# Kernel optimization log

Measured on AMD Instinct MI355X. Metric: run time of the kernel, lower is better.

## Reference

```python
import jax, jax.numpy as jnp
import numpy as np

H = 256; S = 64; AN = 16; D = 8; HH = 8; WW = 8; T = 32; N = 64; NV = 32
HG = 2 + 3 * H  # GRU hidden = sum(parser_sections) = 1 + 1 + 3*H


def _gru(x, w_ih, w_hh, b_ih, b_hh):
    """torch-style GRU over leading axis; x: [L, N, Hin] -> [L, N, HG]."""
    def step(h, xt):
        gi = xt @ w_ih.T + b_ih
        gh = h @ w_hh.T + b_hh
        ir, iz, inn = jnp.split(gi, 3, axis=-1)
        hr, hz, hn = jnp.split(gh, 3, axis=-1)
        r = jax.nn.sigmoid(ir + hr)
        z = jax.nn.sigmoid(iz + hz)
        n = jnp.tanh(inn + r * hn)
        h2 = (1 - z) * n + z * h
        return h2, h2
    h0 = jnp.zeros((x.shape[1], w_hh.shape[1]), x.dtype)
    _, ys = jax.lax.scan(step, h0, x)
    return ys


def _cos(e, m):  # e [N,H], m [N,S,H] -> [N,S]; matches F.cosine_similarity eps=1e-8
    num = jnp.einsum('nh,nsh->ns', e, m)
    den = jnp.linalg.norm(e, axis=-1)[:, None] * jnp.linalg.norm(m, axis=-1)
    return num / jnp.maximum(den, 1e-8)


def _l1norm(x):  # F.normalize(x, p=1, dim=-1)
    return x / jnp.maximum(jnp.abs(x).sum(-1, keepdims=True), 1e-12)


def setup_inputs():
    key = jax.random.key(0)
    ks = jax.random.split(key, 16)
    sc = lambda k, shape, fan: jax.random.normal(k, shape, jnp.float32) / np.float32(np.sqrt(fan))
    return dict(
        base=jax.random.normal(ks[0], (T, N, D, HH, WW), jnp.float32),
        interactable=(jax.random.uniform(ks[1], (T, N, AN - 5)) < 0.5).astype(jnp.float32),
        rnn_hxs=jnp.zeros((1, N, 1 + AN + 1 + H + S), jnp.float32),
        emb=sc(ks[2], (NV, H), 1.0),
        gru_w_ih=sc(ks[3], (3 * HG, H), H),
        gru_w_hh=sc(ks[4], (3 * HG, HG), HG),
        gru_b_ih=jnp.zeros((3 * HG,), jnp.float32),
        gru_b_hh=jnp.zeros((3 * HG,), jnp.float32),
        conv0_w=sc(ks[5], (H, D * H), D * H),
        conv0_b=jnp.zeros((H,), jnp.float32),
        convs_w=sc(ks[6], (2, H, H), H),
        convs_b=jnp.zeros((2, H), jnp.float32),
        lin_w=sc(ks[7], (H, H * HH * WW), H * HH * WW),
        lin_b=jnp.zeros((H,), jnp.float32),
        psi_w=sc(ks[8], (H, H * AN), H * AN),
        psi_b=jnp.zeros((H,), jnp.float32),
        actor_w=sc(ks[9], (AN, H), H),
        actor_b=jnp.zeros((AN,), jnp.float32),
        critic_w=sc(ks[10], (1, H), H),
        critic_b=jnp.zeros((1,), jnp.float32),
        subtasks=jax.random.randint(ks[11], (N, S), 0, NV),
        actions=jax.random.randint(ks[12], (T, N), 0, AN),
    )


def reference(base, interactable, rnn_hxs, emb, gru_w_ih, gru_w_hh, gru_b_ih, gru_b_hh,
              conv0_w, conv0_b, convs_w, convs_b, lin_w, lin_b, psi_w, psi_b,
              actor_w, actor_b, critic_w, critic_b, subtasks, actions):
    # --- parser: GRU over the subtask token sequence ---
    rnn_in = emb[subtasks].transpose(1, 0, 2)                                    # [S, N, H]
    X = _gru(rnn_in, gru_w_ih, gru_w_hh, gru_b_ih, gru_b_hh).transpose(1, 0, 2)  # [N, S, HG]
    c, p0 = X[..., 0], X[..., 1]                                                 # [N, S]
    M = X[..., 2:2 + H]
    Mm = X[..., 2 + H:2 + 2 * H]
    Mp = X[..., 2 + 2 * H:]
    hx = rnn_hxs[0]
    new_ep = jnp.all(rnn_hxs == 0, axis=-1)[0]                                   # [N]
    p_init = jnp.where(new_ep[:, None], p0, hx[:, 1 + AN + 1 + H:])

    def f_net(base_t, r):
        n = base_t.shape[0]
        # outer product [N,H,d,h,w] -> [N, H*d, h, w], then 1x1 convs
        x = (base_t[:, None] * r[:, :, None, None, None]).reshape(n, H * D, HH, WW)
        x = jax.nn.relu(jnp.einsum('nchw,oc->nohw', x, conv0_w) + conv0_b[None, :, None, None])
        for i in range(convs_w.shape[0]):
            x = jax.nn.relu(jnp.einsum('nchw,oc->nohw', x, convs_w[i]) + convs_b[i][None, :, None, None])
        return jax.nn.relu(x.reshape(n, -1) @ lin_w.T + lin_b)

    def step(p, xs):
        base_t, inter_t, a_t = xs
        ps = jax.nn.softmax(p, axis=-1)
        r = jnp.einsum('ns,nsh->nh', ps, M)                                      # memory read
        s = f_net(base_t, r)
        dprobs = jax.nn.softmax(s @ actor_w.T + actor_b, axis=-1)
        nonzero = jnp.pad(inter_t, ((0, 0), (5, 0)), constant_values=1.0)        # [N, AN]
        probs = dprobs * nonzero
        deficit = 1.0 - probs.sum(-1, keepdims=True)
        probs = probs + _l1norm(nonzero) * deficit
        probs = _l1norm(jnp.clip(probs, 0.0, 1.0))
        a_oh = jax.nn.one_hot(a_t, AN, dtype=s.dtype)
        e = (s[:, :, None] * a_oh[:, None, :]).reshape(s.shape[0], H * AN) @ psi_w.T + psi_b
        p_new = ps + c * _cos(e, Mp) - c * _cos(e, Mm)                           # memory write
        v = s @ critic_w.T + critic_b
        out = jnp.concatenate([a_t[:, None].astype(s.dtype), probs, v, s, p_new], axis=-1)
        return p_new, out

    _, hx_out = jax.lax.scan(step, p_init, (base, interactable, actions))        # [T, N, 338]
    return hx_out, hx_out[-1:]
```

## Files before the change

kernel.cpp:

```cpp
#include <hip/hip_runtime.h>
#include <math.h>

constexpr int cH  = 256;
constexpr int cS  = 64;
constexpr int cAN = 16;
constexpr int cD  = 8;
constexpr int cT  = 32;
constexpr int cN  = 64;
constexpr int cHG = 770;
constexpr int cG3 = 2310;
constexpr int cOW = 338;
constexpr int XLD = 800;
constexpr int GLD = 832;
constexpr int MLD = 2496;

__global__ __launch_bounds__(256) void k_gitab(const float* __restrict__ emb,
                                               const float* __restrict__ w_ih,
                                               const float* __restrict__ b_ih,
                                               float* __restrict__ gitp) {
  int v = blockIdx.y;
  int j = blockIdx.x * 256 + threadIdx.x;
  __shared__ float es[cH];
  es[threadIdx.x] = emb[v * cH + threadIdx.x];
  __syncthreads();
  if (j < cG3) {
    float acc = b_ih[j];
    const float* wr = w_ih + (size_t)j * cH;
    #pragma unroll 8
    for (int h = 0; h < cH; ++h) acc += wr[h] * es[h];
    int g = j / cHG, kk = j - g * cHG;
    gitp[(size_t)v * MLD + g * GLD + kk] = acc;
  }
}

__global__ __launch_bounds__(256) void k_wpad(const float* __restrict__ whh,
                                              float* __restrict__ wpadG) {
  int idx = blockIdx.x * 256 + threadIdx.x;
  if (idx < MLD * XLD) {
    int row = idx / XLD, col = idx - row * XLD;
    int g = row / GLD, k = row - g * GLD;
    wpadG[idx] = (k < cHG && col < cHG) ? whh[(size_t)(g * cHG + k) * cHG + col] : 0.f;
  }
}

__global__ __launch_bounds__(256) void k_psiperm(const float* __restrict__ psi_w,
                                                 float* __restrict__ psip) {
  int idx = blockIdx.x * 256 + threadIdx.x;
  int a = idx >> 16, h = (idx >> 8) & 255, o = idx & 255;
  psip[idx] = psi_w[((size_t)o * cH + h) * cAN + a];
}

__global__ __launch_bounds__(256) void k_gru_gemm(const float* __restrict__ wpadG,
                                                  const float* __restrict__ X,
                                                  float* __restrict__ part, int s) {
  int tid = threadIdx.x;
  int tile = blockIdx.x % 39;
  int ks   = blockIdx.x / 39;
  int g = tile / 13, kt = tile - g * 13;
  int cbase = (ks <= 2) ? ks * 13 : 38;
  int ccnt  = (ks < 2) ? 13 : 12;
  int kbase = cbase * 16;
  int csz = ccnt * 16;

  __shared__ float Bst[208][68];
  __shared__ float As[2][16][68];

  const float* bsrc = wpadG + ((size_t)(g * GLD + kt * 64)) * XLD + kbase;
  for (int i = tid; i < 64 * 208; i += 256) {
    int jl = i / 208, k2l = i - jl * 208;
    if (k2l < csz) Bst[k2l][jl] = bsrc[(size_t)jl * XLD + k2l];
  }

  int tm = tid & 15, tj = tid >> 4;
  int lrow = tid >> 2, lcol = (tid & 3) * 4;
  __syncthreads();

  float acc[4][4] = {};
  const float* Xp = X + ((size_t)lrow * cS + (s - 1)) * XLD + kbase;
  float4 av = *(const float4*)(Xp + lcol);
  for (int c = 0; c < ccnt; ++c) {
    int buf = c & 1;
    As[buf][lcol + 0][lrow] = av.x;
    As[buf][lcol + 1][lrow] = av.y;
    As[buf][lcol + 2][lrow] = av.z;
    As[buf][lcol + 3][lrow] = av.w;
    __syncthreads();
    if (c + 1 < ccnt) av = *(const float4*)(Xp + (c + 1) * 16 + lcol);
    #pragma unroll
    for (int kk = 0; kk < 16; ++kk) {
      float4 a4 = *(const float4*)&As[buf][kk][tm * 4];
      float4 b4 = *(const float4*)&Bst[c * 16 + kk][tj * 4];
      acc[0][0] += a4.x * b4.x; acc[0][1] += a4.x * b4.y; acc[0][2] += a4.x * b4.z; acc[0][3] += a4.x * b4.w;
      acc[1][0] += a4.y * b4.x; acc[1][1] += a4.y * b4.y; acc[1][2] += a4.y * b4.z; acc[1][3] += a4.y * b4.w;
      acc[2][0] += a4.z * b4.x; acc[2][1] += a4.z * b4.y; acc[2][2] += a4.z * b4.z; acc[2][3] += a4.z * b4.w;
      acc[3][0] += a4.w * b4.x; acc[3][1] += a4.w * b4.y; acc[3][2] += a4.w * b4.z; acc[3][3] += a4.w * b4.w;
    }
    __syncthreads();
  }
  float* pw = part + (size_t)ks * (64 * MLD) + (size_t)(g * GLD + kt * 64);
  #pragma unroll
  for (int i = 0; i < 4; ++i) {
    *(float4*)(pw + (size_t)(tm * 4 + i) * MLD + tj * 4) =
        make_float4(acc[i][0], acc[i][1], acc[i][2], acc[i][3]);
  }
}

__global__ __launch_bounds__(256) void k_gru_gate(const float* __restrict__ part,
                                                  const float* __restrict__ bhh,
                                                  const float* __restrict__ gitp,
                                                  const int* __restrict__ subtasks,
                                                  float* __restrict__ X, int s) {
  int kq = blockIdx.x, m = blockIdx.y, tid = threadIdx.x;
  if (tid >= 200) return;
  int k = kq * 200 + tid;
  float* xrow = X + ((size_t)m * cS + s) * XLD;
  if (k >= cHG) { xrow[k] = 0.f; return; }
  float accr = 0.f, accz = 0.f, accn = 0.f;
  if (s > 0) {
    const float* pm = part + (size_t)m * MLD;
    #pragma unroll
    for (int q = 0; q < 4; ++q) {
      const float* pq = pm + (size_t)q * (64 * MLD);
      accr += pq[k];
      accz += pq[GLD + k];
      accn += pq[2 * GLD + k];
    }
  }
  int v = subtasks[m * cS + s];
  const float* git = gitp + (size_t)v * MLD;
  float rg = 1.f / (1.f + expf(-(git[k]           + accr + bhh[k])));
  float zg = 1.f / (1.f + expf(-(git[GLD + k]     + accz + bhh[cHG + k])));
  float ng = tanhf(git[2 * GLD + k] + rg * (accn + bhh[2 * cHG + k]));
  float hp = (s > 0) ? X[((size_t)m * cS + (s - 1)) * XLD + k] : 0.f;
  xrow[k] = (1.f - zg) * ng + zg * hp;
}

__global__ __launch_bounds__(256) void k_pinit(const float* __restrict__ hxs,
                                               const float* __restrict__ X,
                                               float* __restrict__ psb,
                                               float* __restrict__ r,
                                               float* __restrict__ nMp,
                                               float* __restrict__ nMm) {
  int n = blockIdx.x, tid = threadIdx.x;
  __shared__ int anynz;
  __shared__ float pss[cS];
  __shared__ float mx, sm;
  if (tid == 0) anynz = 0;
  __syncthreads();
  int nz = (hxs[n * cOW + tid] != 0.f) ? 1 : 0;
  if (tid + 256 < cOW) nz |= (hxs[n * cOW + tid + 256] != 0.f) ? 1 : 0;
  if (nz) anynz = 1;
  __syncthreads();
  bool newep = (anynz == 0);
  if (tid < cS) {
    const float* xr = X + ((size_t)n * cS + tid) * XLD;
    float p0 = xr[1];
    float pv = newep ? p0 : hxs[n * cOW + 1 + cAN + 1 + cH + tid];
    pss[tid] = pv;
    float sp = 0.f, smn = 0.f;
    for (int h = 0; h < cH; ++h) {
      float vp = xr[2 + 2 * cH + h]; sp += vp * vp;
      float vm = xr[2 + cH + h];     smn += vm * vm;
    }
    nMp[n * cS + tid] = sqrtf(sp);
    nMm[n * cS + tid] = sqrtf(smn);
  }
  __syncthreads();
  if (tid == 0) { float m = pss[0]; for (int i = 1; i < cS; ++i) m = fmaxf(m, pss[i]); mx = m; }
  __syncthreads();
  if (tid < cS) pss[tid] = expf(pss[tid] - mx);
  __syncthreads();
  if (tid == 0) { float s = 0.f; for (int i = 0; i < cS; ++i) s += pss[i]; sm = s; }
  __syncthreads();
  if (tid < cS) { pss[tid] /= sm; psb[n * cS + tid] = pss[tid]; }
  __syncthreads();
  float acc = 0.f;
  for (int s2 = 0; s2 < cS; ++s2)
    acc += pss[s2] * X[((size_t)n * cS + s2) * XLD + 2 + tid];
  r[n * cH + tid] = acc;
}

__global__ __launch_bounds__(256) void k_conv0(const float* __restrict__ r,
                                               const float* __restrict__ base,
                                               const float* __restrict__ cw,
                                               const float* __restrict__ cb,
                                               float* __restrict__ x1, int t) {
  int ob = blockIdx.x, n = blockIdx.y, tid = threadIdx.x;
  __shared__ float rs[cH];
  __shared__ float bs[cD * 64];
  __shared__ float wt[32][260];
  __shared__ float w0s[32][9];
  rs[tid] = r[n * cH + tid];
  bs[tid]       = base[((size_t)t * cN + n) * cD * 64 + tid];
  bs[tid + 256] = base[((size_t)t * cN + n) * cD * 64 + tid + 256];
  __syncthreads();
  int o_l = tid >> 3, d = tid & 7;
  float acc = 0.f;
  for (int hc = 0; hc < 8; ++hc) {
    #pragma unroll
    for (int q = 0; q < 8; ++q) {
      int idx = q * 256 + tid;
      int row = idx >> 6, c4 = (idx & 63) * 4;
      *(float4*)&wt[row][c4] =
          *(const float4*)(cw + (size_t)(ob * 32 + row) * (cD * cH) + hc * 256 + c4);
    }
    __syncthreads();
    #pragma unroll
    for (int h2 = 0; h2 < 32; ++h2)
      acc += wt[o_l][h2 * 8 + d] * rs[hc * 32 + h2];
    __syncthreads();
  }
  w0s[o_l][d] = acc;
  __syncthreads();
  int o2 = tid & 31, ijg = tid >> 5;
  float bias = cb[ob * 32 + o2];
  #pragma unroll
  for (int q = 0; q < 8; ++q) {
    int ij = ijg * 8 + q;
    float v = bias;
    #pragma unroll
    for (int d2 = 0; d2 < 8; ++d2) v += w0s[o2][d2] * bs[d2 * 64 + ij];
    x1[((size_t)n * 64 + ij) * cH + ob * 32 + o2] = fmaxf(v, 0.f);
  }
}

__global__ __launch_bounds__(256) void k_gemm_conv(const float* __restrict__ A,
                                                   const float* __restrict__ W,
                                                   const float* __restrict__ bias,
                                                   float* __restrict__ C, int mode) {
  int nb = blockIdx.x, mb = blockIdx.y, tid = threadIdx.x;
  int tm = tid & 15, tj = tid >> 4;
  __shared__ float As[16][68];
  __shared__ float Bs[16][68];
  float acc[4][4] = {{0.f}};
  int lrow = tid >> 2, lcol = (tid & 3) * 4;
  for (int kc = 0; kc < cH; kc += 16) {
    float4 av = *(const float4*)(A + (size_t)(mb * 64 + lrow) * cH + kc + lcol);
    float4 wv = *(const float4*)(W + (size_t)(nb * 64 + lrow) * cH + kc + lcol);
    As[lcol][lrow] = av.x; As[lcol + 1][lrow] = av.y; As[lcol + 2][lrow] = av.z; As[lcol + 3][lrow] = av.w;
    Bs[lcol][lrow] = wv.x; Bs[lcol + 1][lrow] = wv.y; Bs[lcol + 2][lrow] = wv.z; Bs[lcol + 3][lrow] = wv.w;
    __syncthreads();
    #pragma unroll
    for (int kk = 0; kk < 16; ++kk) {
      float4 a4 = *(const float4*)&As[kk][tm * 4];
      float4 b4 = *(const float4*)&Bs[kk][tj * 4];
      acc[0][0] += a4.x * b4.x; acc[0][1] += a4.x * b4.y; acc[0][2] += a4.x * b4.z; acc[0][3] += a4.x * b4.w;
      acc[1][0] += a4.y * b4.x; acc[1][1] += a4.y * b4.y; acc[1][2] += a4.y * b4.z; acc[1][3] += a4.y * b4.w;
      acc[2][0] += a4.z * b4.x; acc[2][1] += a4.z * b4.y; acc[2][2] += a4.z * b4.z; acc[2][3] += a4.z * b4.w;
      acc[3][0] += a4.w * b4.x; acc[3][1] += a4.w * b4.y; acc[3][2] += a4.w * b4.z; acc[3][3] += a4.w * b4.w;
    }
    __syncthreads();
  }
  if (mode == 0) {
    #pragma unroll
    for (int i = 0; i < 4; ++i) {
      int m = mb * 64 + tm * 4 + i;
      float4 o4;
      o4.x = fmaxf(acc[i][0] + bias[nb * 64 + tj * 4 + 0], 0.f);
      o4.y = fmaxf(acc[i][1] + bias[nb * 64 + tj * 4 + 1], 0.f);
      o4.z = fmaxf(acc[i][2] + bias[nb * 64 + tj * 4 + 2], 0.f);
      o4.w = fmaxf(acc[i][3] + bias[nb * 64 + tj * 4 + 3], 0.f);
      *(float4*)(C + (size_t)m * cH + nb * 64 + tj * 4) = o4;
    }
  } else {
    #pragma unroll
    for (int j = 0; j < 4; ++j) {
      int o = nb * 64 + tj * 4 + j;
      float bv = bias[o];
      float4 o4;
      o4.x = fmaxf(acc[0][j] + bv, 0.f);
      o4.y = fmaxf(acc[1][j] + bv, 0.f);
      o4.z = fmaxf(acc[2][j] + bv, 0.f);
      o4.w = fmaxf(acc[3][j] + bv, 0.f);
      *(float4*)(C + (size_t)mb * (64 * cH) + (size_t)o * 64 + tm * 4) = o4;
    }
  }
}

__global__ __launch_bounds__(256) void k_lin(const float* __restrict__ A,
                                             const float* __restrict__ W,
                                             float* __restrict__ part) {
  int nb = blockIdx.x, kcb = blockIdx.y, tid = threadIdx.x;
  int tm = tid & 15, tj = tid >> 4;
  __shared__ float As[16][68];
  __shared__ float Bs[16][68];
  float acc[4][4] = {{0.f}};
  int lrow = tid >> 2, lcol = (tid & 3) * 4;
  for (int kc = 0; kc < 256; kc += 16) {
    float4 av = *(const float4*)(A + (size_t)lrow * 16384 + kcb * 256 + kc + lcol);
    float4 wv = *(const float4*)(W + (size_t)(nb * 64 + lrow) * 16384 + kcb * 256 + kc + lcol);
    As[lcol][lrow] = av.x; As[lcol + 1][lrow] = av.y; As[lcol + 2][lrow] = av.z; As[lcol + 3][lrow] = av.w;
    Bs[lcol][lrow] = wv.x; Bs[lcol + 1][lrow] = wv.y; Bs[lcol + 2][lrow] = wv.z; Bs[lcol + 3][lrow] = wv.w;
    __syncthreads();
    #pragma unroll
    for (int kk = 0; kk < 16; ++kk) {
      float4 a4 = *(const float4*)&As[kk][tm * 4];
      float4 b4 = *(const float4*)&Bs[kk][tj * 4];
      acc[0][0] += a4.x * b4.x; acc[0][1] += a4.x * b4.y; acc[0][2] += a4.x * b4.z; acc[0][3] += a4.x * b4.w;
      acc[1][0] += a4.y * b4.x; acc[1][1] += a4.y * b4.y; acc[1][2] += a4.y * b4.z; acc[1][3] += a4.y * b4.w;
      acc[2][0] += a4.z * b4.x; acc[2][1] += a4.z * b4.y; acc[2][2] += a4.z * b4.z; acc[2][3] += a4.z * b4.w;
      acc[3][0] += a4.w * b4.x; acc[3][1] += a4.w * b4.y; acc[3][2] += a4.w * b4.z; acc[3][3] += a4.w * b4.w;
    }
    __syncthreads();
  }
  #pragma unroll
  for (int i = 0; i < 4; ++i) {
    int n = tm * 4 + i;
    float4 o4 = make_float4(acc[i][0], acc[i][1], acc[i][2], acc[i][3]);
    *(float4*)(part + ((size_t)kcb * cN + n) * cH + nb * 64 + tj * 4) = o4;
  }
}

__global__ __launch_bounds__(256) void k_tail(const float* __restrict__ part,
                                              const float* __restrict__ lin_b,
                                              const float* __restrict__ actor_w,
                                              const float* __restrict__ actor_b,
                                              const float* __restrict__ critic_w,
                                              const float* __restrict__ critic_b,
                                              const float* __restrict__ psip,
                                              const float* __restrict__ psi_b,
                                              const float* __restrict__ inter,
                                              const int* __restrict__ actions,
                                              const float* __restrict__ X,
                                              const float* __restrict__ nMp,
                                              const float* __restrict__ nMm,
                                              float* __restrict__ psb,
                                              float* __restrict__ r,
                                              float* __restrict__ out, int t) {
  int n = blockIdx.x, tid = threadIdx.x;
  __shared__ float ss[cH];
  __shared__ float es[cH];
  __shared__ float lg[cAN], dp[cAN], nzv[cAN], prb[cAN];
  __shared__ float red[256];
  __shared__ float enorm_s;
  __shared__ float pns[cS];
  __shared__ float mx2, sm2;
  float* orow = out + ((size_t)t * cN + n) * cOW;
  float acc = lin_b[tid];
  for (int kc = 0; kc < 64; ++kc) acc += part[((size_t)kc * cN + n) * cH + tid];
  float sv = fmaxf(acc, 0.f);
  ss[tid] = sv;
  orow[1 + cAN + 1 + tid] = sv;
  __syncthreads();
  if (tid < cAN) {
    float a = actor_b[tid];
    const float* wr = actor_w + tid * cH;
    for (int h = 0; h < cH; ++h) a += wr[h] * ss[h];
    lg[tid] = a;
  }
  __syncthreads();
  if (tid < cAN) {
    float m = lg[0];
    for (int i = 1; i < cAN; ++i) m = fmaxf(m, lg[i]);
    dp[tid] = expf(lg[tid] - m);
  }
  __syncthreads();
  if (tid < cAN) {
    float s = 0.f;
    for (int i = 0; i < cAN; ++i) s += dp[i];
    float dprob = dp[tid] / s;
    float nv = (tid < 5) ? 1.f : inter[((size_t)t * cN + n) * (cAN - 5) + (tid - 5)];
    nzv[tid] = nv;
    prb[tid] = dprob * nv;
  }
  __syncthreads();
  if (tid < cAN) {
    float sp = 0.f, sn = 0.f;
    for (int i = 0; i < cAN; ++i) { sp += prb[i]; sn += nzv[i]; }
    float deficit = 1.f - sp;
    float v2 = prb[tid] + (nzv[tid] / fmaxf(sn, 1e-12f)) * deficit;
    prb[tid] = fminf(fmaxf(v2, 0.f), 1.f);
  }
  __syncthreads();
  if (tid < cAN) {
    float s = 0.f;
    for (int i = 0; i < cAN; ++i) s += prb[i];
    orow[1 + tid] = prb[tid] / fmaxf(s, 1e-12f);
  }
  int at = actions[t * cN + n];
  {
    float a = psi_b[tid];
    for (int h = 0; h < cH; ++h) a += psip[((size_t)at * cH + h) * cH + tid] * ss[h];
    es[tid] = a;
    red[tid] = a * a;
  }
  __syncthreads();
  for (int st = 128; st > 0; st >>= 1) {
    if (tid < st) red[tid] += red[tid + st];
    __syncthreads();
  }
  if (tid == 0) enorm_s = sqrtf(red[0]);
  __syncthreads();
  float enorm = enorm_s;
  if (tid == 0) {
    float a = critic_b[0];
    for (int h = 0; h < cH; ++h) a += critic_w[h] * ss[h];
    orow[1 + cAN] = a;
    orow[0] = (float)at;
  }
  if (tid < cS) {
    const float* xr = X + ((size_t)n * cS + tid) * XLD;
    float dpp = 0.f, dmm = 0.f;
    for (int h = 0; h < cH; ++h) {
      float ev = es[h];
      dpp += ev * xr[2 + 2 * cH + h];
      dmm += ev * xr[2 + cH + h];
    }
    float cP = dpp / fmaxf(enorm * nMp[n * cS + tid], 1e-8f);
    float cM = dmm / fmaxf(enorm * nMm[n * cS + tid], 1e-8f);
    float cc = xr[0];
    float pn = psb[n * cS + tid] + cc * cP - cc * cM;
    pns[tid] = pn;
    orow[1 + cAN + 1 + cH + tid] = pn;
  }
  __threadfence_block();
  __syncthreads();
  if (t == cT - 1) {
    float* orow2 = out + (size_t)cT * cN * cOW + (size_t)n * cOW;
    orow2[tid] = orow[tid];
    if (tid + 256 < cOW) orow2[tid + 256] = orow[tid + 256];
  }
  if (tid == 0) { float m2 = pns[0]; for (int i = 1; i < cS; ++i) m2 = fmaxf(m2, pns[i]); mx2 = m2; }
  __syncthreads();
  if (tid < cS) pns[tid] = expf(pns[tid] - mx2);
  __syncthreads();
  if (tid == 0) { float s2 = 0.f; for (int i = 0; i < cS; ++i) s2 += pns[i]; sm2 = s2; }
  __syncthreads();
  if (tid < cS) { pns[tid] /= sm2; psb[n * cS + tid] = pns[tid]; }
  __syncthreads();
  float acc2 = 0.f;
  for (int s2 = 0; s2 < cS; ++s2)
    acc2 += pns[s2] * X[((size_t)n * cS + s2) * XLD + 2 + tid];
  r[n * cH + tid] = acc2;
}

extern "C" void kernel_launch(void* const* d_in, const int* in_sizes, int n_in,
                              void* d_out, int out_size, void* d_ws, size_t ws_size,
                              hipStream_t stream) {
  const float* base     = (const float*)d_in[0];
  const float* inter    = (const float*)d_in[1];
  const float* hxs      = (const float*)d_in[2];
  const float* emb      = (const float*)d_in[3];
  const float* w_ih     = (const float*)d_in[4];
  const float* w_hh     = (const float*)d_in[5];
  const float* b_ih     = (const float*)d_in[6];
  const float* b_hh     = (const float*)d_in[7];
  const float* conv0_w  = (const float*)d_in[8];
  const float* conv0_b  = (const float*)d_in[9];
  const float* convs_w  = (const float*)d_in[10];
  const float* convs_b  = (const float*)d_in[11];
  const float* lin_w    = (const float*)d_in[12];
  const float* lin_b    = (const float*)d_in[13];
  const float* psi_w    = (const float*)d_in[14];
  const float* psi_b    = (const float*)d_in[15];
  const float* actor_w  = (const float*)d_in[16];
  const float* actor_b  = (const float*)d_in[17];
  const float* critic_w = (const float*)d_in[18];
  const float* critic_b = (const float*)d_in[19];
  const int*   subtasks = (const int*)d_in[20];
  const int*   actions  = (const int*)d_in[21];
  float* out = (float*)d_out;
  float* ws  = (float*)d_ws;

  float* gitp  = ws + 0;
  float* psb   = ws + 0;
  float* r     = ws + 4096;
  float* nMp   = ws + 20480;
  float* nMm   = ws + 24576;
  float* X     = ws + 79872;
  float* wpadG = ws + 3356672;
  float* psip  = ws + 3356672;
  float* x1    = ws + 4405248;
  float* part  = x1;
  float* partG = ws + 5353472;
  float* x2    = ws + 5453824;
  float* x3t   = ws + 6502400;

  k_gitab<<<dim3(10, 32), 256, 0, stream>>>(emb, w_ih, b_ih, gitp);
  k_wpad<<<7800, 256, 0, stream>>>(w_hh, wpadG);
  k_gru_gate<<<dim3(4, 64), 256, 0, stream>>>(partG, b_hh, gitp, subtasks, X, 0);
  for (int s = 1; s < cS; ++s) {
    k_gru_gemm<<<156, 256, 0, stream>>>(wpadG, X, partG, s);
    k_gru_gate<<<dim3(4, 64), 256, 0, stream>>>(partG, b_hh, gitp, subtasks, X, s);
  }
  k_psiperm<<<4096, 256, 0, stream>>>(psi_w, psip);
  k_pinit<<<64, 256, 0, stream>>>(hxs, X, psb, r, nMp, nMm);
  for (int t = 0; t < cT; ++t) {
    k_conv0<<<dim3(8, 64), 256, 0, stream>>>(r, base, conv0_w, conv0_b, x1, t);
    k_gemm_conv<<<dim3(4, 64), 256, 0, stream>>>(x1, convs_w, convs_b, x2, 0);
    k_gemm_conv<<<dim3(4, 64), 256, 0, stream>>>(x2, convs_w + 65536, convs_b + 256, x3t, 1);
    k_lin<<<dim3(4, 64), 256, 0, stream>>>(x3t, lin_w, part);
    k_tail<<<64, 256, 0, stream>>>(part, lin_b, actor_w, actor_b, critic_w, critic_b,
                                   psip, psi_b, inter, actions, X, nMp, nMm,
                                   psb, r, out, t);
  }
}
```

Measured before the change: 4.765 ms.

## Restructure conv0 per output channel and store conv activations transposed

Replaces the conv0 kernel with one block per output channel that computes the per-depth weights for all batch items from r held in shared memory, then writes x1 in a transposed [channel][n*64+pixel] layout. The 1x1 conv GEMMs now read the transposed A with coalesced float4 loads and no scatter into shared memory, and the first one also writes transposed output. The tail kernel parallelises the actor and critic dot products across all threads instead of a few serial threads. Costs include a 66KB shared-memory tile in the front kernel, which limits occupancy, and conv weights read directly from global memory.

```diff
diff --git a/kernel.cpp b/kernel.cpp
--- a/kernel.cpp
+++ b/kernel.cpp
@@ -180,64 +180,84 @@
   r[n * cH + tid] = acc;
 }
 
-__global__ __launch_bounds__(256) void k_conv0(const float* __restrict__ r,
+__global__ __launch_bounds__(256) void k_front(const float* __restrict__ r,
                                                const float* __restrict__ base,
                                                const float* __restrict__ cw,
                                                const float* __restrict__ cb,
-                                               float* __restrict__ x1, int t) {
-  int ob = blockIdx.x, n = blockIdx.y, tid = threadIdx.x;
-  __shared__ float rs[cH];
-  __shared__ float bs[cD * 64];
-  __shared__ float wt[32][260];
-  __shared__ float w0s[32][9];
-  rs[tid] = r[n * cH + tid];
-  bs[tid]       = base[((size_t)t * cN + n) * cD * 64 + tid];
-  bs[tid + 256] = base[((size_t)t * cN + n) * cD * 64 + tid + 256];
-  __syncthreads();
-  int o_l = tid >> 3, d = tid & 7;
-  float acc = 0.f;
-  for (int hc = 0; hc < 8; ++hc) {
-    #pragma unroll
-    for (int q = 0; q < 8; ++q) {
-      int idx = q * 256 + tid;
-      int row = idx >> 6, c4 = (idx & 63) * 4;
-      *(float4*)&wt[row][c4] =
-          *(const float4*)(cw + (size_t)(ob * 32 + row) * (cD * cH) + hc * 256 + c4);
-    }
-    __syncthreads();
-    #pragma unroll
-    for (int h2 = 0; h2 < 32; ++h2)
-      acc += wt[o_l][h2 * 8 + d] * rs[hc * 32 + h2];
-    __syncthreads();
-  }
-  w0s[o_l][d] = acc;
-  __syncthreads();
-  int o2 = tid & 31, ijg = tid >> 5;
-  float bias = cb[ob * 32 + o2];
+                                               float* __restrict__ x1T, int t) {
+  int o = blockIdx.x, tid = threadIdx.x;
+  __shared__ float rsQ[64][65][4];
+  __shared__ float w0s[64][9];
+
   #pragma unroll
-  for (int q = 0; q < 8; ++q) {
-    int ij = ijg * 8 + q;
-    float v = bias;
-    #pragma unroll
-    for (int d2 = 0; d2 < 8; ++d2) v += w0s[o2][d2] * bs[d2 * 64 + ij];
-    x1[((size_t)n * 64 + ij) * cH + ob * 32 + o2] = fmaxf(v, 0.f);
-  }
-}
-
-__global__ __launch_bounds__(256) void k_gemm_conv(const float* __restrict__ A,
-                                                   const float* __restrict__ W,
-                                                   const float* __restrict__ bias,
-                                                   float* __restrict__ C, int mode) {
+  for (int it = 0; it < 16; ++it) {
+    int flat4 = it * 256 + tid;
+    int n = flat4 >> 6, hq = flat4 & 63;
+    float4 v = *(const float4*)(r + n * cH + hq * 4);
+    *(float4*)&rsQ[hq][n][0] = v;
+  }
+  __syncthreads();
+
+  {
+    int dg = tid >> 6, n = tid & 63;
+    int d0 = dg * 2;
+    const float* cwo = cw + (size_t)o * (cD * cH);
+    float acc0 = 0.f, acc1 = 0.f;
+    #pragma unroll 4
+    for (int hq = 0; hq < 64; ++hq) {
+      float4 rv = *(const float4*)&rsQ[hq][n][0];
+      #pragma unroll
+      for (int j = 0; j < 4; ++j) {
+        float2 w = *(const float2*)(cwo + (hq * 4 + j) * 8 + d0);
+        float rvj = ((const float*)&rv)[j];
+        acc0 += w.x * rvj;
+        acc1 += w.y * rvj;
+      }
+    }
+    w0s[n][d0]     = acc0;
+    w0s[n][d0 + 1] = acc1;
+  }
+  __syncthreads();
+
+  {
+    int q = tid >> 6, n = tid & 63;
+    float w0[8];
+    #pragma unroll
+    for (int d = 0; d < 8; ++d) w0[d] = w0s[n][d];
+    float bias = cb[o];
+    const float4* b4 = (const float4*)(base + ((size_t)(t * cN + n) * cD) * 64);
+    float* dst = x1T + (size_t)o * 4096 + n * 64 + q * 16;
+    #pragma unroll
+    for (int k = 0; k < 4; ++k) {
+      float4 acc = make_float4(bias, bias, bias, bias);
+      #pragma unroll
+      for (int d = 0; d < 8; ++d) {
+        float4 bv = b4[d * 16 + q * 4 + k];
+        acc.x += w0[d] * bv.x; acc.y += w0[d] * bv.y;
+        acc.z += w0[d] * bv.z; acc.w += w0[d] * bv.w;
+      }
+      acc.x = fmaxf(acc.x, 0.f); acc.y = fmaxf(acc.y, 0.f);
+      acc.z = fmaxf(acc.z, 0.f); acc.w = fmaxf(acc.w, 0.f);
+      *(float4*)(dst + k * 4) = acc;
+    }
+  }
+}
+
+__global__ __launch_bounds__(256) void k_gemmT(const float* __restrict__ AT,
+                                               const float* __restrict__ W,
+                                               const float* __restrict__ bias,
+                                               float* __restrict__ C, int mode) {
   int nb = blockIdx.x, mb = blockIdx.y, tid = threadIdx.x;
   int tm = tid & 15, tj = tid >> 4;
   __shared__ float As[16][68];
   __shared__ float Bs[16][68];
   float acc[4][4] = {{0.f}};
   int lrow = tid >> 2, lcol = (tid & 3) * 4;
+  int kr = tid >> 4, mc4 = (tid & 15) * 4;
   for (int kc = 0; kc < cH; kc += 16) {
-    float4 av = *(const float4*)(A + (size_t)(mb * 64 + lrow) * cH + kc + lcol);
+    float4 av = *(const float4*)(AT + (size_t)(kc + kr) * 4096 + mb * 64 + mc4);
     float4 wv = *(const float4*)(W + (size_t)(nb * 64 + lrow) * cH + kc + lcol);
-    As[lcol][lrow] = av.x; As[lcol + 1][lrow] = av.y; As[lcol + 2][lrow] = av.z; As[lcol + 3][lrow] = av.w;
+    *(float4*)&As[kr][mc4] = av;
     Bs[lcol][lrow] = wv.x; Bs[lcol + 1][lrow] = wv.y; Bs[lcol + 2][lrow] = wv.z; Bs[lcol + 3][lrow] = wv.w;
     __syncthreads();
     #pragma unroll
@@ -253,14 +273,15 @@
   }
   if (mode == 0) {
     #pragma unroll
-    for (int i = 0; i < 4; ++i) {
-      int m = mb * 64 + tm * 4 + i;
+    for (int j = 0; j < 4; ++j) {
+      int o = nb * 64 + tj * 4 + j;
+      float bv = bias[o];
       float4 o4;
-      o4.x = fmaxf(acc[i][0] + bias[nb * 64 + tj * 4 + 0], 0.f);
-      o4.y = fmaxf(acc[i][1] + bias[nb * 64 + tj * 4 + 1], 0.f);
-      o4.z = fmaxf(acc[i][2] + bias[nb * 64 + tj * 4 + 2], 0.f);
-      o4.w = fmaxf(acc[i][3] + bias[nb * 64 + tj * 4 + 3], 0.f);
-      *(float4*)(C + (size_t)m * cH + nb * 64 + tj * 4) = o4;
+      o4.x = fmaxf(acc[0][j] + bv, 0.f);
+      o4.y = fmaxf(acc[1][j] + bv, 0.f);
+      o4.z = fmaxf(acc[2][j] + bv, 0.f);
+      o4.w = fmaxf(acc[3][j] + bv, 0.f);
+      *(float4*)(C + (size_t)o * 4096 + mb * 64 + tm * 4) = o4;
     }
   } else {
     #pragma unroll
@@ -332,6 +353,7 @@
   __shared__ float es[cH];
   __shared__ float lg[cAN], dp[cAN], nzv[cAN], prb[cAN];
   __shared__ float red[256];
+  __shared__ float ared[16][17];
   __shared__ float enorm_s;
   __shared__ float pns[cS];
   __shared__ float mx2, sm2;
@@ -342,10 +364,20 @@
   ss[tid] = sv;
   orow[1 + cAN + 1 + tid] = sv;
   __syncthreads();
+  {
+    int a = tid & 15, hg = tid >> 4;
+    float pa = 0.f;
+    const float* wr = actor_w + a * cH + hg * 16;
+    const float* sh = &ss[hg * 16];
+    #pragma unroll
+    for (int hh2 = 0; hh2 < 16; ++hh2) pa += wr[hh2] * sh[hh2];
+    ared[a][hg] = pa;
+  }
+  __syncthreads();
   if (tid < cAN) {
     float a = actor_b[tid];
-    const float* wr = actor_w + tid * cH;
-    for (int h = 0; h < cH; ++h) a += wr[h] * ss[h];
+    #pragma unroll
+    for (int i = 0; i < 16; ++i) a += ared[tid][i];
     lg[tid] = a;
   }
   __syncthreads();
@@ -392,10 +424,14 @@
   if (tid == 0) enorm_s = sqrtf(red[0]);
   __syncthreads();
   float enorm = enorm_s;
+  red[tid] = critic_w[tid] * ss[tid];
+  __syncthreads();
+  for (int st = 128; st > 0; st >>= 1) {
+    if (tid < st) red[tid] += red[tid + st];
+    __syncthreads();
+  }
   if (tid == 0) {
-    float a = critic_b[0];
-    for (int h = 0; h < cH; ++h) a += critic_w[h] * ss[h];
-    orow[1 + cAN] = a;
+    orow[1 + cAN] = red[0] + critic_b[0];
     orow[0] = (float)at;
   }
   if (tid < cS) {
@@ -470,10 +506,10 @@
   float* X     = ws + 79872;
   float* wpadG = ws + 3356672;
   float* psip  = ws + 3356672;
-  float* x1    = ws + 4405248;
-  float* part  = x1;
+  float* x1T   = ws + 4405248;
+  float* part  = x1T;
   float* partG = ws + 5353472;
-  float* x2    = ws + 5453824;
+  float* x2T   = ws + 5453824;
   float* x3t   = ws + 6502400;
 
   k_gitab<<<dim3(10, 32), 256, 0, stream>>>(emb, w_ih, b_ih, gitp);
@@ -486,9 +522,9 @@
   k_psiperm<<<4096, 256, 0, stream>>>(psi_w, psip);
   k_pinit<<<64, 256, 0, stream>>>(hxs, X, psb, r, nMp, nMm);
   for (int t = 0; t < cT; ++t) {
-    k_conv0<<<dim3(8, 64), 256, 0, stream>>>(r, base, conv0_w, conv0_b, x1, t);
-    k_gemm_conv<<<dim3(4, 64), 256, 0, stream>>>(x1, convs_w, convs_b, x2, 0);
-    k_gemm_conv<<<dim3(4, 64), 256, 0, stream>>>(x2, convs_w + 65536, convs_b + 256, x3t, 1);
+    k_front<<<256, 256, 0, stream>>>(r, base, conv0_w, conv0_b, x1T, t);
+    k_gemmT<<<dim3(4, 64), 256, 0, stream>>>(x1T, convs_w, convs_b, x2T, 0);
+    k_gemmT<<<dim3(4, 64), 256, 0, stream>>>(x2T, convs_w + 65536, convs_b + 256, x3t, 1);
     k_lin<<<dim3(4, 64), 256, 0, stream>>>(x3t, lin_w, part);
     k_tail<<<64, 256, 0, stream>>>(part, lin_b, actor_w, actor_b, critic_w, critic_b,
                                    psip, psi_b, inter, actions, X, nMp, nMm,
```

Measured after the change: 4.732 ms. No clear change (-0.7%).
